# Kernel tuning notes

Hardware: AMD Instinct MI355X
Metric: run time of the kernel (lower is better)

Reference implementation:

```python
import jax, jax.numpy as jnp
import numpy as np

N_EMBD = 768
N_HEAD = 12

def setup_inputs() -> dict:
    key = jax.random.key(0)
    k_x, k_wa, k_ba, k_wp, k_bp = jax.random.split(key, 5)
    C = N_EMBD
    scale = 1.0 / np.sqrt(C)
    return {
        "x": jax.random.normal(k_x, (2, 4096, C), dtype=jnp.float32),
        "W_attn": jax.random.normal(k_wa, (C, 3 * C), dtype=jnp.float32) * scale,
        "b_attn": jax.random.normal(k_ba, (3 * C,), dtype=jnp.float32) * 0.01,
        "W_proj": jax.random.normal(k_wp, (C, C), dtype=jnp.float32) * scale,
        "b_proj": jax.random.normal(k_bp, (C,), dtype=jnp.float32) * 0.01,
    }

def reference(x, W_attn, b_attn, W_proj, b_proj) -> jnp.ndarray:
    B, T, C = x.shape
    H = N_HEAD
    D = C // H  # head dim
    qkv = x @ W_attn + b_attn                     # [B,T,3C]
    q, k, v = jnp.split(qkv, 3, axis=-1)
    # [B,T,C] -> [B,H,T,D]
    q = q.reshape(B, T, H, D).transpose(0, 2, 1, 3)
    k = k.reshape(B, T, H, D).transpose(0, 2, 1, 3)
    v = v.reshape(B, T, H, D).transpose(0, 2, 1, 3)
    scores = jnp.einsum("bhqd,bhkd->bhqk", q, k) * (1.0 / jnp.sqrt(jnp.float32(D)))
    attn = jax.nn.softmax(scores, axis=-1)        # dropout p=0.0 -> identity
    y = jnp.einsum("bhqk,bhkd->bhqd", attn, v)    # [B,H,T,D]
    y = y.transpose(0, 2, 1, 3).reshape(B, T, C)
    return y @ W_proj + b_proj
```

## Files before the change

### kernel.cpp

```cpp
#include <hip/hip_runtime.h>
#include <stdint.h>

#define NB 2
#define NT 4096
#define NC 768
#define NH 12
#define ND 64
#define NBT (NB*NT)
#define NQKV (3*NC)

typedef _Float16 half_t;
typedef __attribute__((ext_vector_type(8))) _Float16 f16x8;
typedef __attribute__((ext_vector_type(4))) _Float16 f16x4;
typedef __attribute__((ext_vector_type(2))) __fp16 fp16x2;
typedef __attribute__((ext_vector_type(4))) float f32x4;

#define MFMA16(a,b,c) __builtin_amdgcn_mfma_f32_16x16x32_f16((a),(b),(c),0,0,0)

__device__ __forceinline__ void load_lds16(const void* g, void* l) {
    auto gp = reinterpret_cast<__attribute__((address_space(1))) char*>(reinterpret_cast<uintptr_t>(g));
    auto lp = reinterpret_cast<__attribute__((address_space(3))) char*>(reinterpret_cast<uintptr_t>(l));
    __builtin_amdgcn_global_load_lds(gp, lp, 16, 0, 0);
}

__global__ __launch_bounds__(256) void k_pack(const float* __restrict__ in, half_t* __restrict__ out, int n4) {
    int i = blockIdx.x * 256 + threadIdx.x;
    if (i >= n4) return;
    float4 f = reinterpret_cast<const float4*>(in)[i];
    f16x4 h;
    h[0] = (half_t)f.x; h[1] = (half_t)f.y; h[2] = (half_t)f.z; h[3] = (half_t)f.w;
    reinterpret_cast<f16x4*>(out)[i] = h;
}

__global__ __launch_bounds__(256) void k_packT(const float* __restrict__ in, half_t* __restrict__ out, int N, int K) {
    int idx = blockIdx.x * 256 + threadIdx.x;
    if (idx >= N * K) return;
    int n = idx / K, k = idx - n * K;
    out[idx] = (half_t)in[(size_t)k * N + n];
}

template<int OUTF32>
__global__ __launch_bounds__(256) void k_gemm(const half_t* __restrict__ A, const half_t* __restrict__ Bt,
                                              const float* __restrict__ bias, void* __restrict__ out, int N) {
    __shared__ half_t As[128 * 32];
    __shared__ half_t Bs[128 * 32];
    const int tid = threadIdx.x;
    const int lane = tid & 63, w = tid >> 6;
    const int m0 = blockIdx.x * 128, n0 = blockIdx.y * 128;
    const int wm = (w >> 1) * 64, wn = (w & 1) * 64;
    const int lr = lane & 15, lk = (lane >> 4) * 8;

    f32x4 acc[4][4];
#pragma unroll
    for (int a = 0; a < 4; ++a)
#pragma unroll
        for (int bq = 0; bq < 4; ++bq) acc[a][bq] = (f32x4){0.f, 0.f, 0.f, 0.f};

    const int c0 = tid, c1 = 256 + tid;
    const int ldsbase = (tid & ~63) * 16;

    for (int ks = 0; ks < 24; ++ks) {
        const int k0 = ks * 32;
        __syncthreads();
        load_lds16(A  + (size_t)(m0 + (c0 >> 2)) * NC + k0 + (c0 & 3) * 8, (char*)As + ldsbase);
        load_lds16(Bt + (size_t)(n0 + (c0 >> 2)) * NC + k0 + (c0 & 3) * 8, (char*)Bs + ldsbase);
        load_lds16(A  + (size_t)(m0 + (c1 >> 2)) * NC + k0 + (c1 & 3) * 8, (char*)As + 4096 + ldsbase);
        load_lds16(Bt + (size_t)(n0 + (c1 >> 2)) * NC + k0 + (c1 & 3) * 8, (char*)Bs + 4096 + ldsbase);
        __syncthreads();
        f16x8 af[4], bf[4];
#pragma unroll
        for (int mi = 0; mi < 4; ++mi)
            af[mi] = *reinterpret_cast<const f16x8*>(&As[(wm + mi * 16 + lr) * 32 + lk]);
#pragma unroll
        for (int ni = 0; ni < 4; ++ni)
            bf[ni] = *reinterpret_cast<const f16x8*>(&Bs[(wn + ni * 16 + lr) * 32 + lk]);
#pragma unroll
        for (int mi = 0; mi < 4; ++mi)
#pragma unroll
            for (int ni = 0; ni < 4; ++ni)
                acc[mi][ni] = MFMA16(af[mi], bf[ni], acc[mi][ni]);
    }

    const int rg = (lane >> 4) * 4;
#pragma unroll
    for (int ni = 0; ni < 4; ++ni) {
        const int gn = n0 + wn + ni * 16 + lr;
        const float bv = bias[gn];
#pragma unroll
        for (int mi = 0; mi < 4; ++mi)
#pragma unroll
            for (int i = 0; i < 4; ++i) {
                const size_t gm = (size_t)(m0 + wm + mi * 16 + rg + i);
                const float v = acc[mi][ni][i] + bv;
                if (OUTF32) reinterpret_cast<float*>(out)[gm * N + gn] = v;
                else        reinterpret_cast<half_t*>(out)[gm * N + gn] = (half_t)v;
            }
    }
}

__global__ __launch_bounds__(256) void k_vt(const half_t* __restrict__ qkv, half_t* __restrict__ Vt) {
    __shared__ half_t tile[64][72];
    const int tid = threadIdx.x;
    const int t0 = blockIdx.x * 64, bh = blockIdx.y;
    const int b = bh / NH, h = bh - b * NH;
    {
        const int tl = tid >> 2, dc = (tid & 3) * 16;
        const half_t* src = qkv + (size_t)(b * NT + t0 + tl) * NQKV + 2 * NC + h * ND + dc;
        f16x8 v0 = *reinterpret_cast<const f16x8*>(src);
        f16x8 v1 = *reinterpret_cast<const f16x8*>(src + 8);
        *reinterpret_cast<f16x8*>(&tile[tl][dc]) = v0;
        *reinterpret_cast<f16x8*>(&tile[tl][dc + 8]) = v1;
    }
    __syncthreads();
    {
        const int d = tid >> 2, tc = (tid & 3) * 16;
        half_t* dst = Vt + ((size_t)bh * ND + d) * NT + t0 + tc;
        f16x8 o0, o1;
#pragma unroll
        for (int j = 0; j < 8; ++j) o0[j] = tile[tc + j][d];
#pragma unroll
        for (int j = 0; j < 8; ++j) o1[j] = tile[tc + 8 + j][d];
        *reinterpret_cast<f16x8*>(dst) = o0;
        *reinterpret_cast<f16x8*>(dst + 8) = o1;
    }
}

__global__ __launch_bounds__(256, 3) void k_attn(const half_t* __restrict__ qkv, const half_t* __restrict__ Vt,
                                                 half_t* __restrict__ Y) {
    __shared__ half_t Kb[2][64 * 64];
    __shared__ half_t Vb[2][64 * 64];
    const int tid = threadIdx.x, lane = tid & 63, w = tid >> 6;
    const int lr = lane & 15, g = lane >> 4;
    const int qt = blockIdx.x, bh = blockIdx.y;
    const int b = bh / NH, h = bh - b * NH;
    const half_t* Qp = qkv + (size_t)b * NT * NQKV + h * ND;
    const half_t* Kp = Qp + NC;
    const half_t* Vbase = Vt + (size_t)bh * ND * NT;
    const int q0 = qt * 128 + w * 32;

    const int sr = tid >> 3;
    const int colh = (((tid & 7) << 3)) ^ ((sr & 7) << 3);
    const int wub = (tid & ~63) * 16;

    f16x8 aq[2][2];
    const half_t cch = (half_t)(0.125f * 1.4426950408889634f);
#pragma unroll
    for (int qf = 0; qf < 2; ++qf)
#pragma unroll
        for (int dh = 0; dh < 2; ++dh) {
            aq[qf][dh] = *reinterpret_cast<const f16x8*>(&Qp[(size_t)(q0 + qf * 16 + lr) * NQKV + dh * 32 + g * 8]);
#pragma unroll
            for (int j = 0; j < 8; ++j) aq[qf][dh][j] = aq[qf][dh][j] * cch;
        }

    const int swk = (lr & 7) << 3;
    const int cA = (g * 8) ^ swk;
    const int cB = (32 + g * 8) ^ swk;
    const int psw = lr & 7;
    const int goff = (g & 1) << 2;
    const int vc[2][2] = { { (((g >> 1) + 0) ^ psw) * 8 + goff, (((g >> 1) + 2) ^ psw) * 8 + goff },
                           { (((g >> 1) + 4) ^ psw) * 8 + goff, (((g >> 1) + 6) ^ psw) * 8 + goff } };

    f32x4 y[2][4];
#pragma unroll
    for (int qf = 0; qf < 2; ++qf)
#pragma unroll
        for (int df = 0; df < 4; ++df) y[qf][df] = (f32x4){0.f, 0.f, 0.f, 0.f};
    float l_[2] = {0.f, 0.f};

    auto stage = [&](int buf, const half_t* Ks, const half_t* Vs) {
        char* kdst = (char*)&Kb[buf][0] + wub;
        char* vdst = (char*)&Vb[buf][0] + wub;
        load_lds16(Ks, kdst);
        load_lds16(Ks + (size_t)32 * NQKV, kdst + 4096);
        load_lds16(Vs, vdst);
        load_lds16(Vs + (size_t)32 * NT, vdst + 4096);
    };

    const half_t* ksrc = Kp + (size_t)sr * NQKV + colh;
    const half_t* vsrc = Vbase + (size_t)sr * NT + colh;
    stage(0, ksrc, vsrc);
    ksrc += (size_t)64 * NQKV;
    vsrc += 64;
    __syncthreads();
    int cur = 0;

    for (int t = 0; t < NT / 64; ++t) {
        if (t < NT / 64 - 1) {
            stage(cur ^ 1, ksrc, vsrc);
            ksrc += (size_t)64 * NQKV;
            vsrc += 64;
        }

        f32x4 s[2][4];
#pragma unroll
        for (int st = 0; st < 4; ++st) { s[0][st] = (f32x4){0.f,0.f,0.f,0.f}; s[1][st] = (f32x4){0.f,0.f,0.f,0.f}; }
        const half_t* Kc = &Kb[cur][0];
        __builtin_amdgcn_s_setprio(1);
#pragma unroll
        for (int st = 0; st < 4; ++st) {
            f16x8 bk0 = *reinterpret_cast<const f16x8*>(&Kc[(st * 16 + lr) * 64 + cA]);
            s[0][st] = MFMA16(bk0, aq[0][0], s[0][st]);
            s[1][st] = MFMA16(bk0, aq[1][0], s[1][st]);
            f16x8 bk1 = *reinterpret_cast<const f16x8*>(&Kc[(st * 16 + lr) * 64 + cB]);
            s[0][st] = MFMA16(bk1, aq[0][1], s[0][st]);
            s[1][st] = MFMA16(bk1, aq[1][1], s[1][st]);
        }
        __builtin_amdgcn_s_setprio(0);

        f16x8 pb[2][2];
#pragma unroll
        for (int qf = 0; qf < 2; ++qf) {
            float ps = 0.f;
#pragma unroll
            for (int ks = 0; ks < 2; ++ks) {
                union { f16x8 v; fp16x2 h[4]; } u;
#pragma unroll
                for (int hs = 0; hs < 2; ++hs) {
                    const int st = 2 * ks + hs;
                    const float p0 = __builtin_amdgcn_exp2f(s[qf][st][0]);
                    const float p1 = __builtin_amdgcn_exp2f(s[qf][st][1]);
                    const float p2 = __builtin_amdgcn_exp2f(s[qf][st][2]);
                    const float p3 = __builtin_amdgcn_exp2f(s[qf][st][3]);
                    u.h[2 * hs]     = __builtin_amdgcn_cvt_pkrtz(p0, p1);
                    u.h[2 * hs + 1] = __builtin_amdgcn_cvt_pkrtz(p2, p3);
                    ps += (p0 + p1) + (p2 + p3);
                }
                pb[qf][ks] = u.v;
            }
            l_[qf] += ps;
        }

        const half_t* Vc = &Vb[cur][0];
        __builtin_amdgcn_s_setprio(1);
#pragma unroll
        for (int ks = 0; ks < 2; ++ks)
#pragma unroll
            for (int df = 0; df < 4; ++df) {
                const half_t* vrow = &Vc[(df * 16 + lr) * 64];
                union { f16x8 v; f16x4 q[2]; } va;
                va.q[0] = *reinterpret_cast<const f16x4*>(vrow + vc[ks][0]);
                va.q[1] = *reinterpret_cast<const f16x4*>(vrow + vc[ks][1]);
                y[0][df] = MFMA16(va.v, pb[0][ks], y[0][df]);
                y[1][df] = MFMA16(va.v, pb[1][ks], y[1][df]);
            }
        __builtin_amdgcn_s_setprio(0);

        __syncthreads();
        cur ^= 1;
    }

#pragma unroll
    for (int qf = 0; qf < 2; ++qf) {
        float l = l_[qf];
        l += __shfl_xor(l, 16);
        l += __shfl_xor(l, 32);
        const float rl = 1.f / l;
        half_t* Yp = Y + (size_t)(b * NT + q0 + qf * 16 + lr) * NC + h * ND + g * 4;
#pragma unroll
        for (int df = 0; df < 4; ++df) {
            union { f16x4 v; fp16x2 hh[2]; } o;
            o.hh[0] = __builtin_amdgcn_cvt_pkrtz(y[qf][df][0] * rl, y[qf][df][1] * rl);
            o.hh[1] = __builtin_amdgcn_cvt_pkrtz(y[qf][df][2] * rl, y[qf][df][3] * rl);
            *reinterpret_cast<f16x4*>(Yp + df * 16) = o.v;
        }
    }
}

extern "C" void kernel_launch(void* const* d_in, const int* in_sizes, int n_in,
                              void* d_out, int out_size, void* d_ws, size_t ws_size,
                              hipStream_t stream) {
    const float* x  = (const float*)d_in[0];
    const float* Wa = (const float*)d_in[1];
    const float* ba = (const float*)d_in[2];
    const float* Wp = (const float*)d_in[3];
    const float* bp = (const float*)d_in[4];
    float* out = (float*)d_out;

    char* ws = (char*)d_ws;
    half_t* xh   = (half_t*)ws; ws += (size_t)NBT * NC * 2;
    half_t* Wat  = (half_t*)ws; ws += (size_t)NQKV * NC * 2;
    half_t* Wpt  = (half_t*)ws; ws += (size_t)NC * NC * 2;
    half_t* qkvh = (half_t*)ws; ws += (size_t)NBT * NQKV * 2;
    half_t* vt   = (half_t*)ws; ws += (size_t)NB * NH * ND * NT * 2;
    half_t* yh   = (half_t*)ws; ws += (size_t)NBT * NC * 2;

    k_pack<<<(NBT * NC / 4 + 255) / 256, 256, 0, stream>>>(x, xh, NBT * NC / 4);
    k_packT<<<(NQKV * NC + 255) / 256, 256, 0, stream>>>(Wa, Wat, NQKV, NC);
    k_packT<<<(NC * NC + 255) / 256, 256, 0, stream>>>(Wp, Wpt, NC, NC);
    k_gemm<0><<<dim3(NBT / 128, NQKV / 128), 256, 0, stream>>>(xh, Wat, ba, qkvh, NQKV);
    k_vt<<<dim3(NT / 64, NB * NH), 256, 0, stream>>>(qkvh, vt);
    k_attn<<<dim3(NT / 128, NB * NH), 256, 0, stream>>>(qkvh, vt, yh);
    k_gemm<1><<<dim3(NBT / 128, NC / 128), 256, 0, stream>>>(yh, Wpt, bp, out, NC);
}
```

Measured before the change: 218.1 us.

## Split attention key tiles across two wave groups with LDS reduction

The attention kernel moves from 256 to 512 threads per block. Two groups of four waves each process half of every 64-key tile (32 keys) for the same 128 queries, and their partial outputs and row sums are combined through shared memory at the end. Each thread now issues half the async loads. The aim is more waves in flight to hide latency, at the cost of duplicated Q registers, an extra reduction step, and heavier register-pressure demands from launch bounds of (512, 6).

```diff
diff --git a/kernel.cpp b/kernel.cpp
--- a/kernel.cpp
+++ b/kernel.cpp
@@ -125,21 +125,28 @@
     }
 }
 
-__global__ __launch_bounds__(256, 3) void k_attn(const half_t* __restrict__ qkv, const half_t* __restrict__ Vt,
+struct __align__(16) AttnSmem {
+    union {
+        struct { half_t K[2][64 * 64]; half_t V[2][64 * 64]; } m;
+        struct { float y[4][64][32]; float l[4][64][2]; } r;
+    };
+};
+
+__global__ __launch_bounds__(512, 6) void k_attn(const half_t* __restrict__ qkv, const half_t* __restrict__ Vt,
                                                  half_t* __restrict__ Y) {
-    __shared__ half_t Kb[2][64 * 64];
-    __shared__ half_t Vb[2][64 * 64];
+    __shared__ AttnSmem sm;
     const int tid = threadIdx.x, lane = tid & 63, w = tid >> 6;
+    const int qw = w & 3, kw = w >> 2;
     const int lr = lane & 15, g = lane >> 4;
     const int qt = blockIdx.x, bh = blockIdx.y;
     const int b = bh / NH, h = bh - b * NH;
     const half_t* Qp = qkv + (size_t)b * NT * NQKV + h * ND;
     const half_t* Kp = Qp + NC;
     const half_t* Vbase = Vt + (size_t)bh * ND * NT;
-    const int q0 = qt * 128 + w * 32;
+    const int q0 = qt * 128 + qw * 32;
 
     const int sr = tid >> 3;
-    const int colh = (((tid & 7) << 3)) ^ ((sr & 7) << 3);
+    const int colh = ((tid & 7) << 3) ^ ((sr & 7) << 3);
     const int wub = (tid & ~63) * 16;
 
     f16x8 aq[2][2];
@@ -158,8 +165,8 @@
     const int cB = (32 + g * 8) ^ swk;
     const int psw = lr & 7;
     const int goff = (g & 1) << 2;
-    const int vc[2][2] = { { (((g >> 1) + 0) ^ psw) * 8 + goff, (((g >> 1) + 2) ^ psw) * 8 + goff },
-                           { (((g >> 1) + 4) ^ psw) * 8 + goff, (((g >> 1) + 6) ^ psw) * 8 + goff } };
+    const int vcol[2] = { (((g >> 1) + 4 * kw + 0) ^ psw) * 8 + goff,
+                          (((g >> 1) + 4 * kw + 2) ^ psw) * 8 + goff };
 
     f32x4 y[2][4];
 #pragma unroll
@@ -169,12 +176,8 @@
     float l_[2] = {0.f, 0.f};
 
     auto stage = [&](int buf, const half_t* Ks, const half_t* Vs) {
-        char* kdst = (char*)&Kb[buf][0] + wub;
-        char* vdst = (char*)&Vb[buf][0] + wub;
-        load_lds16(Ks, kdst);
-        load_lds16(Ks + (size_t)32 * NQKV, kdst + 4096);
-        load_lds16(Vs, vdst);
-        load_lds16(Vs + (size_t)32 * NT, vdst + 4096);
+        load_lds16(Ks, (char*)&sm.m.K[buf][0] + wub);
+        load_lds16(Vs, (char*)&sm.m.V[buf][0] + wub);
     };
 
     const half_t* ksrc = Kp + (size_t)sr * NQKV + colh;
@@ -184,6 +187,7 @@
     vsrc += 64;
     __syncthreads();
     int cur = 0;
+    const int stb = 2 * kw;
 
     for (int t = 0; t < NT / 64; ++t) {
         if (t < NT / 64 - 1) {
@@ -192,77 +196,92 @@
             vsrc += 64;
         }
 
-        f32x4 s[2][4];
-#pragma unroll
-        for (int st = 0; st < 4; ++st) { s[0][st] = (f32x4){0.f,0.f,0.f,0.f}; s[1][st] = (f32x4){0.f,0.f,0.f,0.f}; }
-        const half_t* Kc = &Kb[cur][0];
+        f32x4 s[2][2];
+#pragma unroll
+        for (int sl = 0; sl < 2; ++sl) { s[0][sl] = (f32x4){0.f,0.f,0.f,0.f}; s[1][sl] = (f32x4){0.f,0.f,0.f,0.f}; }
+        const half_t* Kc = &sm.m.K[cur][0];
         __builtin_amdgcn_s_setprio(1);
 #pragma unroll
-        for (int st = 0; st < 4; ++st) {
-            f16x8 bk0 = *reinterpret_cast<const f16x8*>(&Kc[(st * 16 + lr) * 64 + cA]);
-            s[0][st] = MFMA16(bk0, aq[0][0], s[0][st]);
-            s[1][st] = MFMA16(bk0, aq[1][0], s[1][st]);
-            f16x8 bk1 = *reinterpret_cast<const f16x8*>(&Kc[(st * 16 + lr) * 64 + cB]);
-            s[0][st] = MFMA16(bk1, aq[0][1], s[0][st]);
-            s[1][st] = MFMA16(bk1, aq[1][1], s[1][st]);
+        for (int sl = 0; sl < 2; ++sl) {
+            const int row = (stb + sl) * 16 + lr;
+            f16x8 bk0 = *reinterpret_cast<const f16x8*>(&Kc[row * 64 + cA]);
+            s[0][sl] = MFMA16(bk0, aq[0][0], s[0][sl]);
+            s[1][sl] = MFMA16(bk0, aq[1][0], s[1][sl]);
+            f16x8 bk1 = *reinterpret_cast<const f16x8*>(&Kc[row * 64 + cB]);
+            s[0][sl] = MFMA16(bk1, aq[0][1], s[0][sl]);
+            s[1][sl] = MFMA16(bk1, aq[1][1], s[1][sl]);
         }
         __builtin_amdgcn_s_setprio(0);
 
-        f16x8 pb[2][2];
+        f16x8 pb[2];
 #pragma unroll
         for (int qf = 0; qf < 2; ++qf) {
             float ps = 0.f;
-#pragma unroll
-            for (int ks = 0; ks < 2; ++ks) {
-                union { f16x8 v; fp16x2 h[4]; } u;
-#pragma unroll
-                for (int hs = 0; hs < 2; ++hs) {
-                    const int st = 2 * ks + hs;
-                    const float p0 = __builtin_amdgcn_exp2f(s[qf][st][0]);
-                    const float p1 = __builtin_amdgcn_exp2f(s[qf][st][1]);
-                    const float p2 = __builtin_amdgcn_exp2f(s[qf][st][2]);
-                    const float p3 = __builtin_amdgcn_exp2f(s[qf][st][3]);
-                    u.h[2 * hs]     = __builtin_amdgcn_cvt_pkrtz(p0, p1);
-                    u.h[2 * hs + 1] = __builtin_amdgcn_cvt_pkrtz(p2, p3);
-                    ps += (p0 + p1) + (p2 + p3);
-                }
-                pb[qf][ks] = u.v;
-            }
+            union { f16x8 v; fp16x2 h[4]; } u;
+#pragma unroll
+            for (int hs = 0; hs < 2; ++hs) {
+                const float p0 = __builtin_amdgcn_exp2f(s[qf][hs][0]);
+                const float p1 = __builtin_amdgcn_exp2f(s[qf][hs][1]);
+                const float p2 = __builtin_amdgcn_exp2f(s[qf][hs][2]);
+                const float p3 = __builtin_amdgcn_exp2f(s[qf][hs][3]);
+                u.h[2 * hs]     = __builtin_amdgcn_cvt_pkrtz(p0, p1);
+                u.h[2 * hs + 1] = __builtin_amdgcn_cvt_pkrtz(p2, p3);
+                ps += (p0 + p1) + (p2 + p3);
+            }
+            pb[qf] = u.v;
             l_[qf] += ps;
         }
 
-        const half_t* Vc = &Vb[cur][0];
+        const half_t* Vc = &sm.m.V[cur][0];
         __builtin_amdgcn_s_setprio(1);
 #pragma unroll
-        for (int ks = 0; ks < 2; ++ks)
-#pragma unroll
-            for (int df = 0; df < 4; ++df) {
-                const half_t* vrow = &Vc[(df * 16 + lr) * 64];
-                union { f16x8 v; f16x4 q[2]; } va;
-                va.q[0] = *reinterpret_cast<const f16x4*>(vrow + vc[ks][0]);
-                va.q[1] = *reinterpret_cast<const f16x4*>(vrow + vc[ks][1]);
-                y[0][df] = MFMA16(va.v, pb[0][ks], y[0][df]);
-                y[1][df] = MFMA16(va.v, pb[1][ks], y[1][df]);
-            }
+        for (int df = 0; df < 4; ++df) {
+            const half_t* vrow = &Vc[(df * 16 + lr) * 64];
+            union { f16x8 v; f16x4 q[2]; } va;
+            va.q[0] = *reinterpret_cast<const f16x4*>(vrow + vcol[0]);
+            va.q[1] = *reinterpret_cast<const f16x4*>(vrow + vcol[1]);
+            y[0][df] = MFMA16(va.v, pb[0], y[0][df]);
+            y[1][df] = MFMA16(va.v, pb[1], y[1][df]);
+        }
         __builtin_amdgcn_s_setprio(0);
 
         __syncthreads();
         cur ^= 1;
     }
 
-#pragma unroll
-    for (int qf = 0; qf < 2; ++qf) {
-        float l = l_[qf];
-        l += __shfl_xor(l, 16);
-        l += __shfl_xor(l, 32);
-        const float rl = 1.f / l;
-        half_t* Yp = Y + (size_t)(b * NT + q0 + qf * 16 + lr) * NC + h * ND + g * 4;
-#pragma unroll
-        for (int df = 0; df < 4; ++df) {
-            union { f16x4 v; fp16x2 hh[2]; } o;
-            o.hh[0] = __builtin_amdgcn_cvt_pkrtz(y[qf][df][0] * rl, y[qf][df][1] * rl);
-            o.hh[1] = __builtin_amdgcn_cvt_pkrtz(y[qf][df][2] * rl, y[qf][df][3] * rl);
-            *reinterpret_cast<f16x4*>(Yp + df * 16) = o.v;
+    if (kw == 1) {
+#pragma unroll
+        for (int qf = 0; qf < 2; ++qf)
+#pragma unroll
+            for (int df = 0; df < 4; ++df) {
+                const int jb = (qf * 16 + df * 4) ^ ((lane & 7) << 2);
+                *reinterpret_cast<f32x4*>(&sm.r.y[qw][lane][jb]) = y[qf][df];
+            }
+        sm.r.l[qw][lane][0] = l_[0];
+        sm.r.l[qw][lane][1] = l_[1];
+    }
+    __syncthreads();
+    if (kw == 0) {
+#pragma unroll
+        for (int qf = 0; qf < 2; ++qf) {
+#pragma unroll
+            for (int df = 0; df < 4; ++df) {
+                const int jb = (qf * 16 + df * 4) ^ ((lane & 7) << 2);
+                const f32x4 yp = *reinterpret_cast<const f32x4*>(&sm.r.y[qw][lane][jb]);
+                y[qf][df] += yp;
+            }
+            float l = l_[qf] + sm.r.l[qw][lane][qf];
+            l += __shfl_xor(l, 16);
+            l += __shfl_xor(l, 32);
+            const float rl = 1.f / l;
+            half_t* Yp = Y + (size_t)(b * NT + q0 + qf * 16 + lr) * NC + h * ND + g * 4;
+#pragma unroll
+            for (int df = 0; df < 4; ++df) {
+                union { f16x4 v; fp16x2 hh[2]; } o;
+                o.hh[0] = __builtin_amdgcn_cvt_pkrtz(y[qf][df][0] * rl, y[qf][df][1] * rl);
+                o.hh[1] = __builtin_amdgcn_cvt_pkrtz(y[qf][df][2] * rl, y[qf][df][3] * rl);
+                *reinterpret_cast<f16x4*>(Yp + df * 16) = o.v;
+            }
         }
     }
 }
@@ -290,6 +309,6 @@
     k_packT<<<(NC * NC + 255) / 256, 256, 0, stream>>>(Wp, Wpt, NC, NC);
     k_gemm<0><<<dim3(NBT / 128, NQKV / 128), 256, 0, stream>>>(xh, Wat, ba, qkvh, NQKV);
     k_vt<<<dim3(NT / 64, NB * NH), 256, 0, stream>>>(qkvh, vt);
-    k_attn<<<dim3(NT / 128, NB * NH), 256, 0, stream>>>(qkvh, vt, yh);
+    k_attn<<<dim3(NT / 128, NB * NH), 512, 0, stream>>>(qkvh, vt, yh);
     k_gemm<1><<<dim3(NBT / 128, NC / 128), 256, 0, stream>>>(yh, Wpt, bp, out, NC);
 }
```

New measurement: 267.6 us. 22.7% more time.
